# Kernel optimization log

Hardware: AMD Instinct MI355X
Metric: run time of the kernel (lower is better)

Reference implementation:

```python
import jax, jax.numpy as jnp
import numpy as np

B, N, D = 512, 100000, 64
TAU = 1e-4            # gumbel-softmax temperature from source
SIM_RATIO = 0.5       # similarity_ratio init kwarg
COS_EPS = 1e-6


def setup_inputs() -> dict:
    key = jax.random.key(0)
    k1, k2, k3, k4, k5 = jax.random.split(key, 5)
    need_replace = jax.random.randint(k1, (B, 2), 0, N, dtype=jnp.int64) if jax.config.jax_enable_x64 else jax.random.randint(k1, (B, 2), 0, N, dtype=jnp.int32)
    union_feature = jax.random.normal(k2, (B, 2 * D), dtype=jnp.float32)
    all_items = jax.random.normal(k3, (N, D), dtype=jnp.float32) * 0.1
    W = jax.random.normal(k4, (D, 2 * D), dtype=jnp.float32) * 0.05
    b = jax.random.normal(k5, (D,), dtype=jnp.float32) * 0.01
    return {"need_replace": need_replace, "union_feature": union_feature,
            "all_items": all_items, "W": W, "b": b}


def _cosine(a, b):
    # torch.nn.CosineSimilarity(dim=1, eps=1e-6): dot / max(||a||*||b||, eps)
    dot = jnp.sum(a * b, axis=1)
    na = jnp.linalg.norm(a, axis=1)
    nb = jnp.linalg.norm(b, axis=1)
    return dot / jnp.maximum(na * nb, COS_EPS)


def reference(need_replace, union_feature, all_items, W, b):
    item_ids = need_replace[:, 1]
    items_emb = all_items[item_ids]                      # [B, D]
    uif = union_feature @ W.T + b                        # [B, D] (nn.Linear)
    score = uif @ all_items.T                            # [B, N]

    # gumbel_softmax(tau=1e-4, hard=True), training branch
    g = jax.random.gumbel(jax.random.key(42), score.shape, dtype=score.dtype)
    y_soft = jax.nn.softmax((score + g) / TAU, axis=-1)  # [B, N]
    idx = jnp.argmax(y_soft, axis=-1)                    # [B]
    y_hard = jax.nn.one_hot(idx, N, dtype=score.dtype)
    P = y_hard + y_soft - jax.lax.stop_gradient(y_soft)  # straight-through hard one-hot

    item_sequence = jnp.arange(N, dtype=score.dtype)[None, :]
    replaceable_items = jnp.sum(P * item_sequence, axis=-1).astype(jnp.int32)
    replaceable_feat = P @ all_items                     # [B, D]

    sim = _cosine(items_emb, replaceable_feat)
    sim = (sim + 1.0) / 2.0                              # regularize_similarity
    labels = jnp.full((B,), SIM_RATIO, dtype=sim.dtype)
    similarity_loss = jnp.mean((sim - labels) ** 2)      # SimilarityMarginLoss (assumed MSE-to-margin)
    return replaceable_items, replaceable_feat, similarity_loss, jnp.mean(sim)
```

## Files before the change

### kernel.cpp

```cpp
#include <hip/hip_runtime.h>
#include <cstdint>

#define NITEMS   100000
#define BROWS    512
#define DDIM     64
#define S_BLOCKS 391
#define IPB      256
#define NCHUNKS  782
#define FB_Y     8
#define OUT_FEAT 512
#define OUT_LOSS (512 + 512 * 64)
#define OUT_MSIM (OUT_LOSS + 1)

#define BITS23_T   8367841u
#define BITS_RAW_T 4284334592u
#define G_TE       6.001f

typedef __attribute__((ext_vector_type(8)))  short  bf16x8;
typedef __attribute__((ext_vector_type(16))) float  f32x16;
typedef unsigned long long u64;
typedef uint32_t u32;

__device__ __forceinline__ u32 threefry_0_42_xor(u32 e) {
    const u32 K1 = 42u;
    const u32 K2 = 0x1BD11BDAu ^ 42u;
    u32 x0 = 0u;
    u32 x1 = e + K1;
#define TFR(r) { x0 += x1; x1 = (x1 << (r)) | (x1 >> (32 - (r))); x1 ^= x0; }
    TFR(13) TFR(15) TFR(26) TFR(6)
    x0 += K1;  x1 += K2 + 1u;
    TFR(17) TFR(29) TFR(16) TFR(24)
    x0 += K2;  x1 += 2u;
    TFR(13) TFR(15) TFR(26) TFR(6)
    x1 += K1 + 3u;
    TFR(17) TFR(29) TFR(16) TFR(24)
    x0 += K1;  x1 += K2 + 4u;
    TFR(13) TFR(15) TFR(26) TFR(6)
    x0 += K2;  x1 += 5u;
#undef TFR
    return x0 ^ x1;
}

__device__ __forceinline__ float gumbel_from_bits(u32 b) {
    float f = __uint_as_float((b >> 9) | 0x3F800000u) - 1.0f;
    f = fmaxf(f, 1.17549435e-38f);
    return -logf(-logf(f));
}

__device__ __forceinline__ u32 order_map(float v) {
    u32 x = __float_as_uint(v);
    return (x & 0x80000000u) ? ~x : (x | 0x80000000u);
}
__device__ __forceinline__ float unpack_val(u64 p) {
    u32 x = (u32)(p >> 32);
    u32 f = (x & 0x80000000u) ? (x & 0x7FFFFFFFu) : ~x;
    return __uint_as_float(f);
}
__device__ __forceinline__ short f32_to_bf16_rne(float f) {
    u32 b = __float_as_uint(f);
    u32 r = (b + 0x7FFFu + ((b >> 16) & 1u)) >> 16;
    return (short)r;
}
__device__ __forceinline__ float bf16_to_f32(short h) {
    return __uint_as_float(((u32)(uint16_t)h) << 16);
}

__global__ void prep_kernel(const float* __restrict__ UF, const float* __restrict__ W,
                            const float* __restrict__ bias, const float* __restrict__ A,
                            float* __restrict__ uif, float* __restrict__ unorm,
                            float* __restrict__ wsAM4, int* __restrict__ cnt) {
    const int t = threadIdx.x, b = blockIdx.x;
    if (b == 0 && t == 0) *cnt = 0;
    if (b < 128) {
        const int row = b * 4 + (t >> 6);
        const int d   = t & 63;
        const float* w = W + d * 128;
        const float* u = UF + row * 128;
        float s = 0.f;
        for (int k = 0; k < 128; k++) s = fmaf(u[k], w[k], s);
        s += bias[d];
        uif[row * 64 + d] = s;
        float q = s * s;
#pragma unroll
        for (int o = 32; o >= 1; o >>= 1) q += __shfl_xor(q, o);
        if (d == 0) unorm[row] = sqrtf(q);
    } else {
        const int item = (b - 128) * 256 + t;
        float q = 0.f;
        if (item < NITEMS) {
            const float4* r = (const float4*)(A + (size_t)item * DDIM);
#pragma unroll
            for (int k = 0; k < 16; k++) {
                float4 x = r[k];
                q = fmaf(x.x, x.x, q); q = fmaf(x.y, x.y, q);
                q = fmaf(x.z, x.z, q); q = fmaf(x.w, x.w, q);
            }
        }
        float n = sqrtf(q);
#pragma unroll
        for (int o = 32; o >= 1; o >>= 1) n = fmaxf(n, __shfl_xor(n, o));
        if ((t & 63) == 0) wsAM4[(b - 128) * 4 + (t >> 6)] = n;
    }
}

__global__ __launch_bounds__(256, 4) void phase1_kernel(
        const float* __restrict__ A, const float* __restrict__ uif,
        u64* __restrict__ wsT1, float* __restrict__ wsB) {
    __shared__ bf16x8 sh_ah[4 * 64];
    __shared__ bf16x8 sh_al[4 * 64];
    const int tid  = threadIdx.x;
    const int lane = tid & 63;
    const int wv   = tid >> 6;
    const int rg   = blockIdx.y;
    const int sb   = blockIdx.x;
    const int itembase = sb * IPB;
    const int ntiles = min(8, (NITEMS - itembase + 31) >> 5);
    const int row   = rg * 128 + wv * 32 + (lane & 31);
    const int khalf = (lane >> 5) * 8;

    bf16x8 uh[4], ul[4];
#pragma unroll
    for (int s = 0; s < 4; s++) {
        const float* src = uif + row * 64 + khalf + 16 * s;
        float4 v0 = *(const float4*)src;
        float4 v1 = *(const float4*)(src + 4);
        float vv[8] = {v0.x, v0.y, v0.z, v0.w, v1.x, v1.y, v1.z, v1.w};
        bf16x8 h, l2;
#pragma unroll
        for (int j = 0; j < 8; j++) {
            short hh = f32_to_bf16_rne(vv[j]);
            float r  = vv[j] - bf16_to_f32(hh);
            h[j] = hh; l2[j] = f32_to_bf16_rne(r);
        }
        uh[s] = h; ul[s] = l2;
    }

    u64 t1p = 0ull; float t1f = -3.0e38f, t2f = -3.0e38f, sm = -3.0e38f;
    const u32 rowbase_e = (u32)row * (u32)NITEMS;

    const int s_i   = tid & 31;
    const int s_c   = tid >> 5;
    const int s_dst = (s_c >> 1) * 64 + s_i + 32 * (s_c & 1);
    const float* s_srcbase = A + (size_t)s_i * 64 + 8 * s_c;

    for (int t = 0; t < ntiles; t++) {
        const int tb = itembase + t * 32;
        __syncthreads();
        {
            const float* src = s_srcbase + (size_t)tb * 64;
            float4 v0 = *(const float4*)src;
            float4 v1 = *(const float4*)(src + 4);
            float vv[8] = {v0.x, v0.y, v0.z, v0.w, v1.x, v1.y, v1.z, v1.w};
            bf16x8 h, l2;
#pragma unroll
            for (int j = 0; j < 8; j++) {
                short hh = f32_to_bf16_rne(vv[j]);
                float r  = vv[j] - bf16_to_f32(hh);
                h[j] = hh; l2[j] = f32_to_bf16_rne(r);
            }
            sh_ah[s_dst] = h; sh_al[s_dst] = l2;
        }
        __syncthreads();

        f32x16 acc;
#pragma unroll
        for (int z = 0; z < 16; z++) acc[z] = 0.0f;
#pragma unroll
        for (int s = 0; s < 4; s++) {
            bf16x8 ah = sh_ah[s * 64 + lane];
            bf16x8 al = sh_al[s * 64 + lane];
            acc = __builtin_amdgcn_mfma_f32_32x32x16_bf16(ah, uh[s], acc, 0, 0, 0);
            acc = __builtin_amdgcn_mfma_f32_32x32x16_bf16(al, uh[s], acc, 0, 0, 0);
            acc = __builtin_amdgcn_mfma_f32_32x32x16_bf16(ah, ul[s], acc, 0, 0, 0);
        }

        const int ib4 = tb + 4 * (lane >> 5);
#pragma unroll
        for (int i = 0; i < 16; i++) {
            const int il   = (i & 3) + 8 * (i >> 2);
            const int item = ib4 + il;
            u32 rb  = threefry_0_42_xor(rowbase_e + (u32)item);
            float s = acc[i];
            sm = fmaxf(sm, s);
            if (rb >= BITS_RAW_T) {
                float g = gumbel_from_bits(rb);
                float v = s + g;
                if (v > t1f) {
                    t2f = t1f; t1f = v;
                    t1p = ((u64)order_map(v) << 32) | (u32)(~(u32)item);
                } else t2f = fmaxf(t2f, v);
            }
        }
    }

    float bnd = fmaxf(t2f, sm + G_TE);
    {
        u64   op = __shfl_xor(t1p, 32);
        float of = __shfl_xor(t1f, 32);
        float ob = __shfl_xor(bnd, 32);
        if (op > t1p) { bnd = fmaxf(fmaxf(bnd, ob), t1f); t1p = op; t1f = of; }
        else          { bnd = fmaxf(fmaxf(bnd, ob), of); }
    }
    if (lane < 32) {
        wsT1[(size_t)row * S_BLOCKS + sb] = t1p;
        wsB [(size_t)row * S_BLOCKS + sb] = bnd;
    }
}

__global__ void merge_kernel(const u64* __restrict__ wsT1, const float* __restrict__ wsB,
                             const float* __restrict__ wsAM4, const float* __restrict__ unorm,
                             u64* __restrict__ packed, int* __restrict__ rowlist,
                             int* __restrict__ cnt, float* __restrict__ out) {
    const int row = blockIdx.x, t = threadIdx.x;
    if (row == 0 && t == 0) { out[OUT_LOSS] = 0.f; out[OUT_MSIM] = 0.f; }
    float am = 0.f;
    for (int i = t; i < S_BLOCKS * 4; i += 64) am = fmaxf(am, wsAM4[i]);
    u64 p1 = 0ull; float f1 = -3.0e38f, f2 = -3.0e38f;
    for (int sbk = t; sbk < S_BLOCKS; sbk += 64) {
        u64   ep = wsT1[(size_t)row * S_BLOCKS + sbk];
        float e2 = wsB [(size_t)row * S_BLOCKS + sbk];
        if (ep > p1) { f2 = fmaxf(fmaxf(f1, e2), f2); p1 = ep; f1 = unpack_val(ep); }
        else         { float v = unpack_val(ep); f2 = fmaxf(f2, fmaxf(v, e2)); }
    }
#pragma unroll
    for (int off = 1; off < 64; off <<= 1) {
        u64   op  = __shfl_xor(p1, off);
        float of1 = __shfl_xor(f1, off);
        float of2 = __shfl_xor(f2, off);
        am = fmaxf(am, __shfl_xor(am, off));
        if (op > p1) { f2 = fmaxf(fmaxf(f1, of2), f2); p1 = op; f1 = of1; }
        else         { f2 = fmaxf(f2, fmaxf(of1, of2)); }
    }
    if (t == 0) {
        float E = 1.5e-4f * unorm[row] * am + 3.0e-5f;
        if (f1 - f2 > 2.0f * E) {
            packed[row] = p1;
        } else {
            packed[row] = 0ull;
            rowlist[atomicAdd(cnt, 1)] = row;
        }
    }
}

__global__ void fallback_kernel(const float* __restrict__ A, const float* __restrict__ uif,
                                const int* __restrict__ rowlist, const int* __restrict__ cnt,
                                u64* __restrict__ packed) {
    __shared__ float As[128 * 65];
    __shared__ float Us[64];
    const int t  = threadIdx.x;
    const int c  = blockIdx.x;
    const int n0 = c * 128;
    const int nitem = min(128, NITEMS - n0);
    const int total = *cnt;
    if ((int)blockIdx.y >= total) return;

    if (t < nitem) {
        const float4* src = (const float4*)(A + (size_t)(n0 + t) * 64);
#pragma unroll
        for (int k4 = 0; k4 < 16; k4++) {
            float4 x = src[k4];
            As[t * 65 + 4 * k4 + 0] = x.x; As[t * 65 + 4 * k4 + 1] = x.y;
            As[t * 65 + 4 * k4 + 2] = x.z; As[t * 65 + 4 * k4 + 3] = x.w;
        }
    }
    for (int li = blockIdx.y; li < total; li += FB_Y) {
        const int row = rowlist[li];
        __syncthreads();
        if (t < 64) Us[t] = uif[row * 64 + t];
        __syncthreads();
        u64 pk = 0ull;
        if (t < nitem) {
            const int item = n0 + t;
            u32 rb  = threefry_0_42_xor((u32)row * (u32)NITEMS + (u32)item);
            float g = gumbel_from_bits(rb);
            float s0 = 0.f, s1 = 0.f;
#pragma unroll
            for (int k8 = 0; k8 < 64; k8 += 8) {
                s0 = fmaf(As[t * 65 + k8 + 0], Us[k8 + 0], s0);
                s0 = fmaf(As[t * 65 + k8 + 1], Us[k8 + 1], s0);
                s0 = fmaf(As[t * 65 + k8 + 2], Us[k8 + 2], s0);
                s0 = fmaf(As[t * 65 + k8 + 3], Us[k8 + 3], s0);
                s1 = fmaf(As[t * 65 + k8 + 4], Us[k8 + 4], s1);
                s1 = fmaf(As[t * 65 + k8 + 5], Us[k8 + 5], s1);
                s1 = fmaf(As[t * 65 + k8 + 6], Us[k8 + 6], s1);
                s1 = fmaf(As[t * 65 + k8 + 7], Us[k8 + 7], s1);
            }
            float v = (s0 + s1) + g;
            pk = ((u64)order_map(v) << 32) | (u32)(~(u32)item);
        }
#pragma unroll
        for (int off = 1; off < 64; off <<= 1) {
            u64 o = __shfl_xor(pk, off);
            pk = (o > pk) ? o : pk;
        }
        if ((t & 63) == 0) atomicMax(&packed[row], pk);
        __syncthreads();
    }
}

__global__ void resolve_kernel(const u64* __restrict__ packed, const float* __restrict__ A,
                               const int* __restrict__ need_replace, float* __restrict__ out) {
    int b = blockIdx.x, lane = threadIdx.x;
    u64 pk = packed[b];
    int idx = (int)(~(u32)(pk & 0xFFFFFFFFull));
    float fr = A[(size_t)idx * DDIM + lane];
    out[OUT_FEAT + b * DDIM + lane] = fr;
    int   item = need_replace[2 * b + 1];
    float fa   = A[(size_t)item * DDIM + lane];
    float dot = fa * fr, na2 = fa * fa, nb2 = fr * fr;
#pragma unroll
    for (int o = 32; o >= 1; o >>= 1) {
        dot += __shfl_down(dot, o);
        na2 += __shfl_down(na2, o);
        nb2 += __shfl_down(nb2, o);
    }
    if (lane == 0) {
        out[b] = (float)idx;
        float denom = fmaxf(sqrtf(na2) * sqrtf(nb2), 1e-6f);
        float sim = (dot / denom + 1.0f) * 0.5f;
        float d = sim - 0.5f;
        atomicAdd(&out[OUT_LOSS], d * d * (1.0f / 512.0f));
        atomicAdd(&out[OUT_MSIM], sim * (1.0f / 512.0f));
    }
}

extern "C" void kernel_launch(void* const* d_in, const int* in_sizes, int n_in,
                              void* d_out, int out_size, void* d_ws, size_t ws_size,
                              hipStream_t stream) {
    (void)in_sizes; (void)n_in; (void)out_size; (void)ws_size;
    const int*   need_replace = (const int*)d_in[0];
    const float* UF           = (const float*)d_in[1];
    const float* A            = (const float*)d_in[2];
    const float* W            = (const float*)d_in[3];
    const float* bias         = (const float*)d_in[4];
    float* out = (float*)d_out;

    char* ws = (char*)d_ws;
    u64*   wsT1    = (u64*)  (ws);
    float* wsB     = (float*)(ws + 1601536);
    float* uif     = (float*)(ws + 2402304);
    u64*   packed  = (u64*)  (ws + 2533376);
    float* unorm   = (float*)(ws + 2537472);
    float* wsAM4   = (float*)(ws + 2539520);
    int*   rowlist = (int*)  (ws + 2545776);
    int*   cnt     = (int*)  (ws + 2547824);

    prep_kernel<<<519, 256, 0, stream>>>(UF, W, bias, A, uif, unorm, wsAM4, cnt);
    phase1_kernel<<<dim3(S_BLOCKS, 4), 256, 0, stream>>>(A, uif, wsT1, wsB);
    merge_kernel<<<BROWS, 64, 0, stream>>>(wsT1, wsB, wsAM4, unorm, packed, rowlist, cnt, out);
    fallback_kernel<<<dim3(NCHUNKS, FB_Y), 128, 0, stream>>>(A, uif, rowlist, cnt, packed);
    resolve_kernel<<<BROWS, 64, 0, stream>>>(packed, A, need_replace, out);
}
```

Measured before the change: 259.3 us.

## Fuse resolve into merge/fallback, prefetch phase1 tiles, use alignbit rotates

Removes the separate resolve kernel. Rows that are decided in merge are finalized there, and fallback rows are finalized by the last chunk block through a per-row done counter with a threadfence. The phase1 main loop now loads the next tile into registers ahead of time, overlapping global loads with the MFMA work. Threefry rotates use alignbit, and the prep linear layer stages W transposed in LDS. Together these save one kernel launch and some latency, at the cost of added atomics and more complex completion logic.

```diff
diff --git a/kernel.cpp b/kernel.cpp
--- a/kernel.cpp
+++ b/kernel.cpp
@@ -12,7 +12,6 @@
 #define OUT_LOSS (512 + 512 * 64)
 #define OUT_MSIM (OUT_LOSS + 1)
 
-#define BITS23_T   8367841u
 #define BITS_RAW_T 4284334592u
 #define G_TE       6.001f
 
@@ -20,22 +19,24 @@
 typedef __attribute__((ext_vector_type(16))) float  f32x16;
 typedef unsigned long long u64;
 typedef uint32_t u32;
+
+#define ROTL(x, r) __builtin_amdgcn_alignbit((x), (x), 32u - (r))
 
 __device__ __forceinline__ u32 threefry_0_42_xor(u32 e) {
     const u32 K1 = 42u;
     const u32 K2 = 0x1BD11BDAu ^ 42u;
     u32 x0 = 0u;
     u32 x1 = e + K1;
-#define TFR(r) { x0 += x1; x1 = (x1 << (r)) | (x1 >> (32 - (r))); x1 ^= x0; }
-    TFR(13) TFR(15) TFR(26) TFR(6)
+#define TFR(r) { x0 += x1; x1 = ROTL(x1, r) ^ x0; }
+    TFR(13u) TFR(15u) TFR(26u) TFR(6u)
     x0 += K1;  x1 += K2 + 1u;
-    TFR(17) TFR(29) TFR(16) TFR(24)
+    TFR(17u) TFR(29u) TFR(16u) TFR(24u)
     x0 += K2;  x1 += 2u;
-    TFR(13) TFR(15) TFR(26) TFR(6)
+    TFR(13u) TFR(15u) TFR(26u) TFR(6u)
     x1 += K1 + 3u;
-    TFR(17) TFR(29) TFR(16) TFR(24)
+    TFR(17u) TFR(29u) TFR(16u) TFR(24u)
     x0 += K1;  x1 += K2 + 4u;
-    TFR(13) TFR(15) TFR(26) TFR(6)
+    TFR(13u) TFR(15u) TFR(26u) TFR(6u)
     x0 += K2;  x1 += 5u;
 #undef TFR
     return x0 ^ x1;
@@ -46,7 +47,6 @@
     f = fmaxf(f, 1.17549435e-38f);
     return -logf(-logf(f));
 }
-
 __device__ __forceinline__ u32 order_map(float v) {
     u32 x = __float_as_uint(v);
     return (x & 0x80000000u) ? ~x : (x | 0x80000000u);
@@ -68,16 +68,26 @@
 __global__ void prep_kernel(const float* __restrict__ UF, const float* __restrict__ W,
                             const float* __restrict__ bias, const float* __restrict__ A,
                             float* __restrict__ uif, float* __restrict__ unorm,
-                            float* __restrict__ wsAM4, int* __restrict__ cnt) {
+                            float* __restrict__ wsAM4, int* __restrict__ cnt,
+                            int* __restrict__ done, float* __restrict__ out) {
     const int t = threadIdx.x, b = blockIdx.x;
-    if (b == 0 && t == 0) *cnt = 0;
+    if (b == 0) {
+        if (t == 0) { *cnt = 0; out[OUT_LOSS] = 0.f; out[OUT_MSIM] = 0.f; }
+        done[t] = 0; done[t + 256] = 0;
+    }
     if (b < 128) {
+        __shared__ float Wt[128 * 65];
+        for (int i = t; i < 8192; i += 256) {
+            int d = i >> 7, k = i & 127;
+            Wt[k * 65 + d] = W[i];
+        }
+        __syncthreads();
         const int row = b * 4 + (t >> 6);
         const int d   = t & 63;
-        const float* w = W + d * 128;
         const float* u = UF + row * 128;
         float s = 0.f;
-        for (int k = 0; k < 128; k++) s = fmaf(u[k], w[k], s);
+#pragma unroll 4
+        for (int k = 0; k < 128; k++) s = fmaf(u[k], Wt[k * 65 + d], s);
         s += bias[d];
         uif[row * 64 + d] = s;
         float q = s * s;
@@ -143,24 +153,29 @@
     const int s_dst = (s_c >> 1) * 64 + s_i + 32 * (s_c & 1);
     const float* s_srcbase = A + (size_t)s_i * 64 + 8 * s_c;
 
+    float4 p0 = *(const float4*)(s_srcbase + (size_t)itembase * 64);
+    float4 p1 = *(const float4*)(s_srcbase + (size_t)itembase * 64 + 4);
+
     for (int t = 0; t < ntiles; t++) {
         const int tb = itembase + t * 32;
-        __syncthreads();
+        bf16x8 h, l2;
         {
-            const float* src = s_srcbase + (size_t)tb * 64;
-            float4 v0 = *(const float4*)src;
-            float4 v1 = *(const float4*)(src + 4);
-            float vv[8] = {v0.x, v0.y, v0.z, v0.w, v1.x, v1.y, v1.z, v1.w};
-            bf16x8 h, l2;
+            float vv[8] = {p0.x, p0.y, p0.z, p0.w, p1.x, p1.y, p1.z, p1.w};
 #pragma unroll
             for (int j = 0; j < 8; j++) {
                 short hh = f32_to_bf16_rne(vv[j]);
                 float r  = vv[j] - bf16_to_f32(hh);
                 h[j] = hh; l2[j] = f32_to_bf16_rne(r);
             }
-            sh_ah[s_dst] = h; sh_al[s_dst] = l2;
-        }
-        __syncthreads();
+        }
+        __syncthreads();
+        sh_ah[s_dst] = h; sh_al[s_dst] = l2;
+        __syncthreads();
+        if (t + 1 < ntiles) {
+            const float* src = s_srcbase + (size_t)(tb + 32) * 64;
+            p0 = *(const float4*)src;
+            p1 = *(const float4*)(src + 4);
+        }
 
         f32x16 acc;
 #pragma unroll
@@ -209,10 +224,10 @@
 
 __global__ void merge_kernel(const u64* __restrict__ wsT1, const float* __restrict__ wsB,
                              const float* __restrict__ wsAM4, const float* __restrict__ unorm,
+                             const float* __restrict__ A, const int* __restrict__ need_replace,
                              u64* __restrict__ packed, int* __restrict__ rowlist,
                              int* __restrict__ cnt, float* __restrict__ out) {
     const int row = blockIdx.x, t = threadIdx.x;
-    if (row == 0 && t == 0) { out[OUT_LOSS] = 0.f; out[OUT_MSIM] = 0.f; }
     float am = 0.f;
     for (int i = t; i < S_BLOCKS * 4; i += 64) am = fmaxf(am, wsAM4[i]);
     u64 p1 = 0ull; float f1 = -3.0e38f, f2 = -3.0e38f;
@@ -231,22 +246,42 @@
         if (op > p1) { f2 = fmaxf(fmaxf(f1, of2), f2); p1 = op; f1 = of1; }
         else         { f2 = fmaxf(f2, fmaxf(of1, of2)); }
     }
-    if (t == 0) {
-        float E = 1.5e-4f * unorm[row] * am + 3.0e-5f;
-        if (f1 - f2 > 2.0f * E) {
-            packed[row] = p1;
-        } else {
-            packed[row] = 0ull;
-            rowlist[atomicAdd(cnt, 1)] = row;
-        }
+    const float E = 1.5e-4f * unorm[row] * am + 3.0e-5f;
+    if (f1 - f2 > 2.0f * E) {
+        const int idx = (int)(~(u32)(p1 & 0xFFFFFFFFull));
+        float fr = A[(size_t)idx * DDIM + t];
+        out[OUT_FEAT + row * DDIM + t] = fr;
+        int   item = need_replace[2 * row + 1];
+        float fa   = A[(size_t)item * DDIM + t];
+        float dot = fa * fr, na2 = fa * fa, nb2 = fr * fr;
+#pragma unroll
+        for (int o = 32; o >= 1; o >>= 1) {
+            dot += __shfl_down(dot, o);
+            na2 += __shfl_down(na2, o);
+            nb2 += __shfl_down(nb2, o);
+        }
+        if (t == 0) {
+            out[row] = (float)idx;
+            float denom = fmaxf(sqrtf(na2) * sqrtf(nb2), 1e-6f);
+            float sim = (dot / denom + 1.0f) * 0.5f;
+            float d = sim - 0.5f;
+            atomicAdd(&out[OUT_LOSS], d * d * (1.0f / 512.0f));
+            atomicAdd(&out[OUT_MSIM], sim * (1.0f / 512.0f));
+        }
+    } else if (t == 0) {
+        packed[row] = 0ull;
+        rowlist[atomicAdd(cnt, 1)] = row;
     }
 }
 
 __global__ void fallback_kernel(const float* __restrict__ A, const float* __restrict__ uif,
                                 const int* __restrict__ rowlist, const int* __restrict__ cnt,
-                                u64* __restrict__ packed) {
+                                const int* __restrict__ need_replace,
+                                u64* __restrict__ packed, int* __restrict__ done,
+                                float* __restrict__ out) {
     __shared__ float As[128 * 65];
     __shared__ float Us[64];
+    __shared__ int   sh_last;
     const int t  = threadIdx.x;
     const int c  = blockIdx.x;
     const int n0 = c * 128;
@@ -295,32 +330,35 @@
         }
         if ((t & 63) == 0) atomicMax(&packed[row], pk);
         __syncthreads();
-    }
-}
-
-__global__ void resolve_kernel(const u64* __restrict__ packed, const float* __restrict__ A,
-                               const int* __restrict__ need_replace, float* __restrict__ out) {
-    int b = blockIdx.x, lane = threadIdx.x;
-    u64 pk = packed[b];
-    int idx = (int)(~(u32)(pk & 0xFFFFFFFFull));
-    float fr = A[(size_t)idx * DDIM + lane];
-    out[OUT_FEAT + b * DDIM + lane] = fr;
-    int   item = need_replace[2 * b + 1];
-    float fa   = A[(size_t)item * DDIM + lane];
-    float dot = fa * fr, na2 = fa * fa, nb2 = fr * fr;
-#pragma unroll
-    for (int o = 32; o >= 1; o >>= 1) {
-        dot += __shfl_down(dot, o);
-        na2 += __shfl_down(na2, o);
-        nb2 += __shfl_down(nb2, o);
-    }
-    if (lane == 0) {
-        out[b] = (float)idx;
-        float denom = fmaxf(sqrtf(na2) * sqrtf(nb2), 1e-6f);
-        float sim = (dot / denom + 1.0f) * 0.5f;
-        float d = sim - 0.5f;
-        atomicAdd(&out[OUT_LOSS], d * d * (1.0f / 512.0f));
-        atomicAdd(&out[OUT_MSIM], sim * (1.0f / 512.0f));
+        if (t == 0) {
+            __threadfence();
+            sh_last = (atomicAdd(&done[li], 1) == NCHUNKS - 1) ? 1 : 0;
+        }
+        __syncthreads();
+        if (sh_last && t < 64) {
+            u64 fin = atomicMax(&packed[row], 0ull);
+            const int idx = (int)(~(u32)(fin & 0xFFFFFFFFull));
+            float fr = A[(size_t)idx * DDIM + t];
+            out[OUT_FEAT + row * DDIM + t] = fr;
+            int   item = need_replace[2 * row + 1];
+            float fa   = A[(size_t)item * DDIM + t];
+            float dot = fa * fr, na2 = fa * fa, nb2 = fr * fr;
+#pragma unroll
+            for (int o = 32; o >= 1; o >>= 1) {
+                dot += __shfl_down(dot, o);
+                na2 += __shfl_down(na2, o);
+                nb2 += __shfl_down(nb2, o);
+            }
+            if (t == 0) {
+                out[row] = (float)idx;
+                float denom = fmaxf(sqrtf(na2) * sqrtf(nb2), 1e-6f);
+                float sim = (dot / denom + 1.0f) * 0.5f;
+                float d = sim - 0.5f;
+                atomicAdd(&out[OUT_LOSS], d * d * (1.0f / 512.0f));
+                atomicAdd(&out[OUT_MSIM], sim * (1.0f / 512.0f));
+            }
+        }
+        __syncthreads();
     }
 }
 
@@ -344,10 +382,12 @@
     float* wsAM4   = (float*)(ws + 2539520);
     int*   rowlist = (int*)  (ws + 2545776);
     int*   cnt     = (int*)  (ws + 2547824);
-
-    prep_kernel<<<519, 256, 0, stream>>>(UF, W, bias, A, uif, unorm, wsAM4, cnt);
+    int*   done    = (int*)  (ws + 2547828);
+
+    prep_kernel<<<519, 256, 0, stream>>>(UF, W, bias, A, uif, unorm, wsAM4, cnt, done, out);
     phase1_kernel<<<dim3(S_BLOCKS, 4), 256, 0, stream>>>(A, uif, wsT1, wsB);
-    merge_kernel<<<BROWS, 64, 0, stream>>>(wsT1, wsB, wsAM4, unorm, packed, rowlist, cnt, out);
-    fallback_kernel<<<dim3(NCHUNKS, FB_Y), 128, 0, stream>>>(A, uif, rowlist, cnt, packed);
-    resolve_kernel<<<BROWS, 64, 0, stream>>>(packed, A, need_replace, out);
-}
+    merge_kernel<<<BROWS, 64, 0, stream>>>(wsT1, wsB, wsAM4, unorm, A, need_replace,
+                                           packed, rowlist, cnt, out);
+    fallback_kernel<<<dim3(NCHUNKS, FB_Y), 128, 0, stream>>>(A, uif, rowlist, cnt,
+                                                             need_replace, packed, done, out);
+}
```

New measurement: 260.6 us. No clear change (+0.5%).
